# Optimization experiments

Hardware: AMD Instinct MI355X
Metric: run time of the kernel (lower is better)

## Reference

```python
import jax, jax.numpy as jnp
import numpy as np

EPS = 1e-9


def setup_inputs() -> dict:
    key = jax.random.key(0)
    k1, k2, k3 = jax.random.split(key, 3)
    B, N, E, F_IN, F_OUT = 8, 2048, 1024, 256, 256
    x = jax.random.normal(k1, (B, N, F_IN), dtype=jnp.float32)
    H = jax.random.uniform(k2, (B, N, E), dtype=jnp.float32)  # soft incidence matrix
    weight = jax.random.normal(k3, (F_IN, F_OUT), dtype=jnp.float32) * (1.0 / np.sqrt(F_OUT))
    return {"x": x, "H": H, "weight": weight}


def reference(x, H, weight):
    # x: [B, N, Fin], H: [B, N, E], weight: [Fin, Fout]
    # Torch builds diag_embed(Dv_inv)/diag_embed(De_inv) and uses dense bmm;
    # mathematically identical to elementwise row-scaling, done here directly.
    Dv = jnp.sum(H, axis=2)                       # [B, N]  (= bmm(H, ones))
    De = jnp.sum(H, axis=1)                       # [B, E]
    Dv_inv = 1.0 / (Dv + EPS)
    De_inv = 1.0 / (De + EPS)
    xw = jnp.matmul(x, weight)                    # [B, N, Fout]
    HTX = jnp.einsum('bne,bnf->bef', H, xw)       # H^T @ X
    HDeHTX = jnp.einsum('bne,bef->bnf', H, De_inv[:, :, None] * HTX)
    out = Dv_inv[:, :, None] * HDeHTX             # [B, N, Fout]
    # dropout in eval mode (identity); relu kept
    return jax.nn.relu(out)
```

## Files before the change

### kernel.cpp

```cpp
#include <hip/hip_runtime.h>
#include <stdint.h>


typedef __bf16 bf16x8 __attribute__((ext_vector_type(8)));
typedef float f32x4 __attribute__((ext_vector_type(4)));

#define PADK 72

__device__ __forceinline__ uint16_t f2b(float f) {
  __bf16 h = (__bf16)f;
  return __builtin_bit_cast(uint16_t, h);
}

__device__ __forceinline__ f32x4 mfma16(bf16x8 a, bf16x8 b, f32x4 c) {
  return __builtin_amdgcn_mfma_f32_16x16x32_bf16(a, b, c, 0, 0, 0);
}

__device__ __forceinline__ void gload16(const void* src, void* dst) {
  __builtin_amdgcn_global_load_lds(
      (const __attribute__((address_space(1))) void*)src,
      (__attribute__((address_space(3))) void*)dst, 16, 0, 0);
}

#define PIPE_WAIT4() do { \
    asm volatile("s_waitcnt vmcnt(4)" ::: "memory"); \
    __builtin_amdgcn_s_barrier(); \
    __builtin_amdgcn_sched_barrier(0); \
  } while (0)
#define PIPE_WAIT0() do { \
    asm volatile("s_waitcnt vmcnt(0)" ::: "memory"); \
    __builtin_amdgcn_s_barrier(); \
    __builtin_amdgcn_sched_barrier(0); \
  } while (0)

__global__ __launch_bounds__(256) void k_prep_w(const float* __restrict__ W,
    uint16_t* __restrict__ Wt) {
  __shared__ __align__(16) uint16_t T[64 * 68];
  const int k0 = blockIdx.x * 64, f0 = blockIdx.y * 64;
  const int t = threadIdx.x;
  const int r0 = (t >> 4) * 4, cc = (t & 15) * 4;
  float vv[4][4];
  #pragma unroll
  for (int i = 0; i < 4; ++i) {
    float4 q = *(const float4*)(W + (size_t)(k0 + r0 + i) * 256 + f0 + cc);
    vv[i][0] = q.x; vv[i][1] = q.y; vv[i][2] = q.z; vv[i][3] = q.w;
  }
  #pragma unroll
  for (int j = 0; j < 4; ++j) {
    union { uint16_t s[4]; uint2 u; } p;
    #pragma unroll
    for (int i = 0; i < 4; ++i) p.s[i] = f2b(vv[i][j]);
    *(uint2*)&T[(cc + j) * 68 + r0] = p.u;
  }
  __syncthreads();
  const int er = t >> 2, c2 = (t & 3) * 16;
  union { uint16_t s[16]; uint4 q[2]; } o;
  #pragma unroll
  for (int m = 0; m < 4; ++m)
    *(uint2*)&o.s[m * 4] = *(const uint2*)&T[er * 68 + c2 + m * 4];
  uint16_t* dst = Wt + (size_t)(f0 + er) * 256 + k0 + c2;
  *(uint4*)dst = o.q[0];
  *(uint4*)(dst + 8) = o.q[1];
}

__global__ __launch_bounds__(256) void k_prep_h(const float* __restrict__ H,
    uint16_t* __restrict__ Hbt, uint16_t* __restrict__ Hb,
    float* __restrict__ DvPart, float* __restrict__ DePart) {
  __shared__ __align__(16) uint16_t T[64 * 68];
  __shared__ float cs[4][64];
  const int n0 = blockIdx.x * 64, e0 = blockIdx.y * 64, b = blockIdx.z;
  const int t = threadIdx.x, lane = t & 63, wave = t >> 6;
  const int r0 = (t >> 4) * 4;
  const int cc = (t & 15) * 4;
  float vv[4][4];
  float dv[4];
  float de0 = 0.f, de1 = 0.f, de2 = 0.f, de3 = 0.f;
  #pragma unroll
  for (int i = 0; i < 4; ++i) {
    float4 q = *(const float4*)(H + ((size_t)b * 2048 + n0 + r0 + i) * 1024 + e0 + cc);
    vv[i][0] = q.x; vv[i][1] = q.y; vv[i][2] = q.z; vv[i][3] = q.w;
    float rs = (q.x + q.y) + (q.z + q.w);
    rs += __shfl_xor(rs, 1); rs += __shfl_xor(rs, 2);
    rs += __shfl_xor(rs, 4); rs += __shfl_xor(rs, 8);
    dv[i] = rs;
    de0 += q.x; de1 += q.y; de2 += q.z; de3 += q.w;
  }
  #pragma unroll
  for (int i = 0; i < 4; ++i) {
    union { uint16_t s[4]; uint2 u; } p;
    #pragma unroll
    for (int j = 0; j < 4; ++j) p.s[j] = f2b(vv[i][j]);
    *(uint2*)(Hb + ((size_t)b * 2048 + n0 + r0 + i) * 1024 + e0 + cc) = p.u;
  }
  #pragma unroll
  for (int j = 0; j < 4; ++j) {
    union { uint16_t s[4]; uint2 u; } p;
    #pragma unroll
    for (int i = 0; i < 4; ++i) p.s[i] = f2b(vv[i][j]);
    *(uint2*)&T[(cc + j) * 68 + r0] = p.u;
  }
  de0 += __shfl_xor(de0, 16); de0 += __shfl_xor(de0, 32);
  de1 += __shfl_xor(de1, 16); de1 += __shfl_xor(de1, 32);
  de2 += __shfl_xor(de2, 16); de2 += __shfl_xor(de2, 32);
  de3 += __shfl_xor(de3, 16); de3 += __shfl_xor(de3, 32);
  if (lane < 16) *(float4*)&cs[wave][cc] = make_float4(de0, de1, de2, de3);
  if ((lane & 15) == 0) {
    #pragma unroll
    for (int i = 0; i < 4; ++i)
      DvPart[((size_t)b * 2048 + n0 + r0 + i) * 16 + blockIdx.y] = dv[i];
  }
  __syncthreads();
  const int er = t >> 2, c2 = (t & 3) * 16;
  union { uint16_t s[16]; uint4 q[2]; } o;
  #pragma unroll
  for (int m = 0; m < 4; ++m)
    *(uint2*)&o.s[m * 4] = *(const uint2*)&T[er * 68 + c2 + m * 4];
  uint16_t* dst = Hbt + ((size_t)b * 1024 + e0 + er) * 2048 + n0 + c2;
  *(uint4*)dst = o.q[0];
  *(uint4*)(dst + 8) = o.q[1];
  if (t < 64) {
    float s = (cs[0][t] + cs[1][t]) + (cs[2][t] + cs[3][t]);
    DePart[((size_t)b * 1024 + e0 + t) * 32 + blockIdx.x] = s;
  }
}

__global__ __launch_bounds__(256) void k_gemm1(const float* __restrict__ X,
    const uint16_t* __restrict__ Wt, uint16_t* __restrict__ XWt) {
  __shared__ __align__(16) uint16_t As[2][128 * 64];
  __shared__ __align__(16) uint16_t Bs[2][64 * PADK];
  const int n0 = blockIdx.x * 64, f0 = blockIdx.y * 128, b = blockIdx.z;
  const int t = threadIdx.x, lane = t & 63, wave = t >> 6;
  const int l15 = lane & 15, lq = lane >> 4;
  const int rlane = lane >> 3;
  const int srcswz = ((lane & 7) ^ rlane) << 3;
  const uint16_t* Ag = Wt + (size_t)f0 * 256;
  const int br = t >> 2, kc = (t & 3) * 16;
  const float* Xg = X + ((size_t)b * 2048 + n0 + br) * 256 + kc;
  float4 RX[4];
  auto stageA = [&](uint16_t* Ad, int kt) {
    const int k0 = kt * 64;
    #pragma unroll
    for (int i = 0; i < 4; ++i) {
      const int r = wave * 32 + i * 8;
      gload16(Ag + (size_t)(r + rlane) * 256 + k0 + srcswz, Ad + r * 64);
    }
  };
  auto gloadB = [&](int kt) {
    const float* s = Xg + kt * 64;
    #pragma unroll
    for (int q = 0; q < 4; ++q) RX[q] = *(const float4*)(s + q * 4);
  };
  auto writeB = [&](uint16_t* Bd) {
    uint16_t* d = Bd + br * PADK + kc;
    const float* f = (const float*)RX;
    #pragma unroll
    for (int q = 0; q < 2; ++q) {
      union { uint16_t s[8]; uint4 u; } p;
      #pragma unroll
      for (int j = 0; j < 8; ++j) p.s[j] = f2b(f[q * 8 + j]);
      *(uint4*)(d + q * 8) = p.u;
    }
  };
  f32x4 acc[4][2] = {};
  auto compute = [&](const uint16_t* Ad, const uint16_t* Bd) {
    #pragma unroll
    for (int h = 0; h < 2; ++h) {
      bf16x8 af[4], bf[2];
      #pragma unroll
      for (int i = 0; i < 4; ++i) {
        const int r = (wave >> 1) * 64 + i * 16 + l15;
        af[i] = *(const bf16x8*)(Ad + r * 64 + ((((h << 2) | lq) ^ (r & 7)) << 3));
      }
      #pragma unroll
      for (int j = 0; j < 2; ++j) {
        const int r = (wave & 1) * 32 + j * 16 + l15;
        bf[j] = *(const bf16x8*)(Bd + r * PADK + h * 32 + lq * 8);
      }
      #pragma unroll
      for (int i = 0; i < 4; ++i)
        #pragma unroll
        for (int j = 0; j < 2; ++j)
          acc[i][j] = mfma16(af[i], bf[j], acc[i][j]);
    }
  };
  stageA(As[0], 0); gloadB(0); writeB(Bs[0]);
  __syncthreads();
  for (int kt = 0; kt < 4; kt += 2) {
    stageA(As[1], kt + 1); gloadB(kt + 1);
    compute(As[0], Bs[0]);
    writeB(Bs[1]);
    __syncthreads();
    if (kt + 2 < 4) { stageA(As[0], kt + 2); gloadB(kt + 2); }
    compute(As[1], Bs[1]);
    if (kt + 2 < 4) writeB(Bs[0]);
    __syncthreads();
  }
  #pragma unroll
  for (int i = 0; i < 4; ++i) {
    const int fr = f0 + (wave >> 1) * 64 + i * 16 + lq * 4;
    #pragma unroll
    for (int j = 0; j < 2; ++j) {
      const int col = n0 + (wave & 1) * 32 + j * 16 + l15;
      #pragma unroll
      for (int reg = 0; reg < 4; ++reg)
        XWt[((size_t)b * 256 + fr + reg) * 2048 + col] = f2b(acc[i][j][reg]);
    }
  }
}

__global__ __launch_bounds__(256) void k_gemm2(const uint16_t* __restrict__ Hbt,
    const uint16_t* __restrict__ XWt, const float* __restrict__ DePart,
    uint16_t* __restrict__ Yt) {
  __shared__ __align__(16) uint16_t As[3][64 * 64];
  __shared__ __align__(16) uint16_t Bs[3][64 * 64];
  __shared__ float sde[64];
  const int e0 = blockIdx.x * 64, f0 = blockIdx.y * 64, b = blockIdx.z;
  const int t = threadIdx.x, lane = t & 63, wave = t >> 6;
  const int l15 = lane & 15, lq = lane >> 4;
  const int rlane = lane >> 3;
  const int srcswz = ((lane & 7) ^ rlane) << 3;
  const uint16_t* Ag = XWt + ((size_t)b * 256 + f0) * 2048;
  const uint16_t* Bg = Hbt + ((size_t)b * 1024 + e0) * 2048;
  auto stage = [&](uint16_t* Ad, uint16_t* Bd, int kt) {
    const int k0 = kt * 64;
    #pragma unroll
    for (int i = 0; i < 2; ++i) {
      const int r = wave * 16 + i * 8;
      gload16(Ag + (size_t)(r + rlane) * 2048 + k0 + srcswz, Ad + r * 64);
      gload16(Bg + (size_t)(r + rlane) * 2048 + k0 + srcswz, Bd + r * 64);
    }
  };
  f32x4 acc[2][2] = {};
  auto compute = [&](const uint16_t* Ad, const uint16_t* Bd) {
    #pragma unroll
    for (int h = 0; h < 2; ++h) {
      bf16x8 af[2], bf[2];
      #pragma unroll
      for (int i = 0; i < 2; ++i) {
        const int r = (wave >> 1) * 32 + i * 16 + l15;
        af[i] = *(const bf16x8*)(Ad + r * 64 + ((((h << 2) | lq) ^ (r & 7)) << 3));
      }
      #pragma unroll
      for (int j = 0; j < 2; ++j) {
        const int r = (wave & 1) * 32 + j * 16 + l15;
        bf[j] = *(const bf16x8*)(Bd + r * 64 + ((((h << 2) | lq) ^ (r & 7)) << 3));
      }
      #pragma unroll
      for (int i = 0; i < 2; ++i)
        #pragma unroll
        for (int j = 0; j < 2; ++j)
          acc[i][j] = mfma16(af[i], bf[j], acc[i][j]);
    }
  };
  if (t < 64) {
    const float* p = DePart + ((size_t)b * 1024 + e0 + t) * 32;
    float4 a0 = *(const float4*)(p + 0),  a1 = *(const float4*)(p + 4);
    float4 a2 = *(const float4*)(p + 8),  a3 = *(const float4*)(p + 12);
    float4 a4 = *(const float4*)(p + 16), a5 = *(const float4*)(p + 20);
    float4 a6 = *(const float4*)(p + 24), a7 = *(const float4*)(p + 28);
    float s = (((a0.x + a0.y) + (a0.z + a0.w)) + ((a1.x + a1.y) + (a1.z + a1.w)))
            + (((a2.x + a2.y) + (a2.z + a2.w)) + ((a3.x + a3.y) + (a3.z + a3.w)))
            + ((((a4.x + a4.y) + (a4.z + a4.w)) + ((a5.x + a5.y) + (a5.z + a5.w)))
            + (((a6.x + a6.y) + (a6.z + a6.w)) + ((a7.x + a7.y) + (a7.z + a7.w))));
    sde[t] = 1.f / (s + 1e-9f);
  }
  stage(As[0], Bs[0], 0);
  stage(As[1], Bs[1], 1);
  __syncthreads();
  const int NT = 32;
  uint16_t *cA = As[0], *nA = As[1], *fA = As[2];
  uint16_t *cB = Bs[0], *nB = Bs[1], *fB = Bs[2];
  for (int kt = 0; kt < NT - 2; ++kt) {
    stage(fA, fB, kt + 2);
    compute(cA, cB);
    PIPE_WAIT4();
    uint16_t* t1 = cA; cA = nA; nA = fA; fA = t1;
    uint16_t* t2 = cB; cB = nB; nB = fB; fB = t2;
  }
  compute(cA, cB);
  PIPE_WAIT0();
  compute(nA, nB);
  #pragma unroll
  for (int i = 0; i < 2; ++i) {
    const int fr = f0 + (wave >> 1) * 32 + i * 16 + lq * 4;
    #pragma unroll
    for (int j = 0; j < 2; ++j) {
      const int el = (wave & 1) * 32 + j * 16 + l15;
      const float sc = sde[el];
      uint16_t* dst = Yt + ((size_t)b * 256 + fr) * 1024 + e0 + el;
      #pragma unroll
      for (int reg = 0; reg < 4; ++reg)
        dst[(size_t)reg * 1024] = f2b(acc[i][j][reg] * sc);
    }
  }
}

__global__ __launch_bounds__(256) void k_gemm3(const uint16_t* __restrict__ Hb,
    const uint16_t* __restrict__ Yt, const float* __restrict__ DvPart,
    float* __restrict__ out) {
  __shared__ __align__(16) uint16_t As[3][64 * 64];
  __shared__ __align__(16) uint16_t Bs[3][64 * 64];
  __shared__ float sdv[64];
  const int n0 = blockIdx.x * 64, f0 = blockIdx.y * 64, b = blockIdx.z;
  const int t = threadIdx.x, lane = t & 63, wave = t >> 6;
  const int l15 = lane & 15, lq = lane >> 4;
  const int rlane = lane >> 3;
  const int srcswz = ((lane & 7) ^ rlane) << 3;
  const uint16_t* Ag = Hb + ((size_t)b * 2048 + n0) * 1024;
  const uint16_t* Bg = Yt + ((size_t)b * 256 + f0) * 1024;
  auto stage = [&](uint16_t* Ad, uint16_t* Bd, int kt) {
    const int k0 = kt * 64;
    #pragma unroll
    for (int i = 0; i < 2; ++i) {
      const int r = wave * 16 + i * 8;
      gload16(Ag + (size_t)(r + rlane) * 1024 + k0 + srcswz, Ad + r * 64);
      gload16(Bg + (size_t)(r + rlane) * 1024 + k0 + srcswz, Bd + r * 64);
    }
  };
  f32x4 acc[2][2] = {};
  auto compute = [&](const uint16_t* Ad, const uint16_t* Bd) {
    #pragma unroll
    for (int h = 0; h < 2; ++h) {
      bf16x8 af[2], bf[2];
      #pragma unroll
      for (int i = 0; i < 2; ++i) {
        const int r = (wave >> 1) * 32 + i * 16 + l15;
        af[i] = *(const bf16x8*)(Ad + r * 64 + ((((h << 2) | lq) ^ (r & 7)) << 3));
      }
      #pragma unroll
      for (int j = 0; j < 2; ++j) {
        const int r = (wave & 1) * 32 + j * 16 + l15;
        bf[j] = *(const bf16x8*)(Bd + r * 64 + ((((h << 2) | lq) ^ (r & 7)) << 3));
      }
      #pragma unroll
      for (int i = 0; i < 2; ++i)
        #pragma unroll
        for (int j = 0; j < 2; ++j)
          acc[i][j] = mfma16(af[i], bf[j], acc[i][j]);
    }
  };
  if (t < 64) {
    const float* p = DvPart + ((size_t)b * 2048 + n0 + t) * 16;
    float4 a0 = *(const float4*)(p + 0),  a1 = *(const float4*)(p + 4);
    float4 a2 = *(const float4*)(p + 8),  a3 = *(const float4*)(p + 12);
    float s = (((a0.x + a0.y) + (a0.z + a0.w)) + ((a1.x + a1.y) + (a1.z + a1.w)))
            + (((a2.x + a2.y) + (a2.z + a2.w)) + ((a3.x + a3.y) + (a3.z + a3.w)));
    sdv[t] = 1.f / (s + 1e-9f);
  }
  stage(As[0], Bs[0], 0);
  stage(As[1], Bs[1], 1);
  __syncthreads();
  const int NT = 16;
  uint16_t *cA = As[0], *nA = As[1], *fA = As[2];
  uint16_t *cB = Bs[0], *nB = Bs[1], *fB = Bs[2];
  for (int kt = 0; kt < NT - 2; ++kt) {
    stage(fA, fB, kt + 2);
    compute(cA, cB);
    PIPE_WAIT4();
    uint16_t* t1 = cA; cA = nA; nA = fA; fA = t1;
    uint16_t* t2 = cB; cB = nB; nB = fB; fB = t2;
  }
  compute(cA, cB);
  PIPE_WAIT0();
  compute(nA, nB);
  #pragma unroll
  for (int i = 0; i < 2; ++i) {
    const int nl = (wave >> 1) * 32 + i * 16 + lq * 4;
    #pragma unroll
    for (int reg = 0; reg < 4; ++reg) {
      const int row = n0 + nl + reg;
      const float sc = sdv[nl + reg];
      #pragma unroll
      for (int j = 0; j < 2; ++j) {
        const int col = f0 + (wave & 1) * 32 + j * 16 + l15;
        const float v = acc[i][j][reg] * sc;
        out[((size_t)b * 2048 + row) * 256 + col] = v > 0.f ? v : 0.f;
      }
    }
  }
}

extern "C" void kernel_launch(void* const* d_in, const int* in_sizes, int n_in,
                              void* d_out, int out_size, void* d_ws, size_t ws_size,
                              hipStream_t stream) {
  (void)in_sizes; (void)n_in; (void)out_size;
  const float* x = (const float*)d_in[0];
  const float* H = (const float*)d_in[1];
  const float* W = (const float*)d_in[2];
  float* out = (float*)d_out;

  if (ws_size < 81920000) return;
  char* ws = (char*)d_ws;
  uint16_t* Hbt    = (uint16_t*)(ws);
  uint16_t* Hb     = (uint16_t*)(ws + 33554432);
  uint16_t* XWt    = (uint16_t*)(ws + 67108864);
  uint16_t* Yt     = (uint16_t*)(ws + 75497472);
  float*    DvPart = (float*)(ws + 79691776);
  float*    DePart = (float*)(ws + 80740352);
  uint16_t* Wt     = (uint16_t*)(ws + 81788928);

  k_prep_w<<<dim3(4, 4),      256, 0, stream>>>(W, Wt);
  k_prep_h<<<dim3(32, 16, 8), 256, 0, stream>>>(H, Hbt, Hb, DvPart, DePart);
  k_gemm1 <<<dim3(32, 2, 8),  256, 0, stream>>>(x, Wt, XWt);
  k_gemm2 <<<dim3(16, 4, 8),  256, 0, stream>>>(Hbt, XWt, DePart, Yt);
  k_gemm3 <<<dim3(32, 4, 8),  256, 0, stream>>>(Hb, Yt, DvPart, out);
}
```

Measured before the change: 79.37 us.

## Enlarge GEMM2 and GEMM3 tiles with K=32 stages and new swizzle

GEMM2 now has each 512-thread block cover the full 256-wide feature dimension for a 64-edge tile, so the H tile is loaded once rather than four times. GEMM3 moves to 128x128 output tiles with 4x4 MFMA accumulators per wave. Both kernels drop the K step to 32 with a matching LDS swizzle and adjust the pipeline wait counts to fit. Operand reuse per global load goes up, but grids shrink a lot: GEMM2 drops to 128 blocks and GEMM3 to 256. That may underfill the GPU's CUs and add latency exposure per block.

```diff
diff --git a/kernel.cpp b/kernel.cpp
--- a/kernel.cpp
+++ b/kernel.cpp
@@ -22,13 +22,8 @@
       (__attribute__((address_space(3))) void*)dst, 16, 0, 0);
 }
 
-#define PIPE_WAIT4() do { \
-    asm volatile("s_waitcnt vmcnt(4)" ::: "memory"); \
-    __builtin_amdgcn_s_barrier(); \
-    __builtin_amdgcn_sched_barrier(0); \
-  } while (0)
-#define PIPE_WAIT0() do { \
-    asm volatile("s_waitcnt vmcnt(0)" ::: "memory"); \
+#define PIPE_WAITN(N) do { \
+    asm volatile("s_waitcnt vmcnt(" #N ")" ::: "memory"); \
     __builtin_amdgcn_s_barrier(); \
     __builtin_amdgcn_sched_barrier(0); \
   } while (0)
@@ -208,49 +203,46 @@
   }
 }
 
-__global__ __launch_bounds__(256) void k_gemm2(const uint16_t* __restrict__ Hbt,
+__global__ __launch_bounds__(512) void k_gemm2(const uint16_t* __restrict__ Hbt,
     const uint16_t* __restrict__ XWt, const float* __restrict__ DePart,
     uint16_t* __restrict__ Yt) {
-  __shared__ __align__(16) uint16_t As[3][64 * 64];
-  __shared__ __align__(16) uint16_t Bs[3][64 * 64];
+  __shared__ __align__(16) uint16_t As[3][256 * 32];
+  __shared__ __align__(16) uint16_t Bs[3][64 * 32];
   __shared__ float sde[64];
-  const int e0 = blockIdx.x * 64, f0 = blockIdx.y * 64, b = blockIdx.z;
+  const int e0 = blockIdx.x * 64, b = blockIdx.z;
   const int t = threadIdx.x, lane = t & 63, wave = t >> 6;
   const int l15 = lane & 15, lq = lane >> 4;
-  const int rlane = lane >> 3;
-  const int srcswz = ((lane & 7) ^ rlane) << 3;
-  const uint16_t* Ag = XWt + ((size_t)b * 256 + f0) * 2048;
+  const int wf = wave >> 1, we = wave & 1;
+  const int ri = lane >> 2, slot = lane & 3;
+  const int ksw = (slot ^ ((ri >> 1) & 3)) * 8;
+  const uint16_t* Ag = XWt + (size_t)b * 256 * 2048;
   const uint16_t* Bg = Hbt + ((size_t)b * 1024 + e0) * 2048;
   auto stage = [&](uint16_t* Ad, uint16_t* Bd, int kt) {
-    const int k0 = kt * 64;
-    #pragma unroll
-    for (int i = 0; i < 2; ++i) {
-      const int r = wave * 16 + i * 8;
-      gload16(Ag + (size_t)(r + rlane) * 2048 + k0 + srcswz, Ad + r * 64);
-      gload16(Bg + (size_t)(r + rlane) * 2048 + k0 + srcswz, Bd + r * 64);
-    }
-  };
-  f32x4 acc[2][2] = {};
+    const int k0 = kt * 32;
+    const int a0 = wave * 2;
+    gload16(Ag + (size_t)(a0 * 16 + ri) * 2048 + k0 + ksw, Ad + a0 * 512);
+    gload16(Ag + (size_t)(a0 * 16 + 16 + ri) * 2048 + k0 + ksw, Ad + (a0 + 1) * 512);
+    const int bb = wave >> 1;
+    gload16(Bg + (size_t)(bb * 16 + ri) * 2048 + k0 + ksw, Bd + bb * 512);
+  };
+  f32x4 acc[4][2] = {};
   auto compute = [&](const uint16_t* Ad, const uint16_t* Bd) {
-    #pragma unroll
-    for (int h = 0; h < 2; ++h) {
-      bf16x8 af[2], bf[2];
-      #pragma unroll
-      for (int i = 0; i < 2; ++i) {
-        const int r = (wave >> 1) * 32 + i * 16 + l15;
-        af[i] = *(const bf16x8*)(Ad + r * 64 + ((((h << 2) | lq) ^ (r & 7)) << 3));
-      }
-      #pragma unroll
-      for (int j = 0; j < 2; ++j) {
-        const int r = (wave & 1) * 32 + j * 16 + l15;
-        bf[j] = *(const bf16x8*)(Bd + r * 64 + ((((h << 2) | lq) ^ (r & 7)) << 3));
-      }
-      #pragma unroll
-      for (int i = 0; i < 2; ++i)
-        #pragma unroll
-        for (int j = 0; j < 2; ++j)
-          acc[i][j] = mfma16(af[i], bf[j], acc[i][j]);
-    }
+    bf16x8 af[4], bf[2];
+    #pragma unroll
+    for (int i = 0; i < 4; ++i) {
+      const int r = wf * 64 + i * 16 + l15;
+      af[i] = *(const bf16x8*)(Ad + r * 32 + ((lq ^ ((r >> 1) & 3)) * 8));
+    }
+    #pragma unroll
+    for (int j = 0; j < 2; ++j) {
+      const int r = we * 32 + j * 16 + l15;
+      bf[j] = *(const bf16x8*)(Bd + r * 32 + ((lq ^ ((r >> 1) & 3)) * 8));
+    }
+    #pragma unroll
+    for (int i = 0; i < 4; ++i)
+      #pragma unroll
+      for (int j = 0; j < 2; ++j)
+        acc[i][j] = mfma16(af[i], bf[j], acc[i][j]);
   };
   if (t < 64) {
     const float* p = DePart + ((size_t)b * 1024 + e0 + t) * 32;
@@ -267,112 +259,110 @@
   stage(As[0], Bs[0], 0);
   stage(As[1], Bs[1], 1);
   __syncthreads();
+  const int NT = 64;
+  uint16_t *cA = As[0], *nA = As[1], *fA = As[2];
+  uint16_t *cB = Bs[0], *nB = Bs[1], *fB = Bs[2];
+  for (int kt = 0; kt < NT - 2; ++kt) {
+    stage(fA, fB, kt + 2);
+    compute(cA, cB);
+    PIPE_WAITN(3);
+    uint16_t* t1 = cA; cA = nA; nA = fA; fA = t1;
+    uint16_t* t2 = cB; cB = nB; nB = fB; fB = t2;
+  }
+  compute(cA, cB);
+  PIPE_WAITN(0);
+  compute(nA, nB);
+  #pragma unroll
+  for (int i = 0; i < 4; ++i) {
+    const int fr = wf * 64 + i * 16 + lq * 4;
+    #pragma unroll
+    for (int j = 0; j < 2; ++j) {
+      const int el = we * 32 + j * 16 + l15;
+      const float sc = sde[el];
+      uint16_t* dst = Yt + ((size_t)b * 256 + fr) * 1024 + e0 + el;
+      #pragma unroll
+      for (int reg = 0; reg < 4; ++reg)
+        dst[(size_t)reg * 1024] = f2b(acc[i][j][reg] * sc);
+    }
+  }
+}
+
+__global__ __launch_bounds__(256) void k_gemm3(const uint16_t* __restrict__ Hb,
+    const uint16_t* __restrict__ Yt, const float* __restrict__ DvPart,
+    float* __restrict__ out) {
+  __shared__ __align__(16) uint16_t As[3][128 * 32];
+  __shared__ __align__(16) uint16_t Bs[3][128 * 32];
+  __shared__ float sdv[128];
+  const int n0 = blockIdx.x * 128, f0 = blockIdx.y * 128, b = blockIdx.z;
+  const int t = threadIdx.x, lane = t & 63, wave = t >> 6;
+  const int l15 = lane & 15, lq = lane >> 4;
+  const int wn = wave >> 1, wf = wave & 1;
+  const int ri = lane >> 2, slot = lane & 3;
+  const int ksw = (slot ^ ((ri >> 1) & 3)) * 8;
+  const uint16_t* Ag = Hb + ((size_t)b * 2048 + n0) * 1024;
+  const uint16_t* Bg = Yt + ((size_t)b * 256 + f0) * 1024;
+  auto stage = [&](uint16_t* Ad, uint16_t* Bd, int kt) {
+    const int k0 = kt * 32;
+    const int c0 = wave * 2;
+    #pragma unroll
+    for (int i = 0; i < 2; ++i) {
+      gload16(Ag + (size_t)((c0 + i) * 16 + ri) * 1024 + k0 + ksw, Ad + (c0 + i) * 512);
+      gload16(Bg + (size_t)((c0 + i) * 16 + ri) * 1024 + k0 + ksw, Bd + (c0 + i) * 512);
+    }
+  };
+  f32x4 acc[4][4] = {};
+  auto compute = [&](const uint16_t* Ad, const uint16_t* Bd) {
+    bf16x8 af[4], bf[4];
+    #pragma unroll
+    for (int i = 0; i < 4; ++i) {
+      const int r = wn * 64 + i * 16 + l15;
+      af[i] = *(const bf16x8*)(Ad + r * 32 + ((lq ^ ((r >> 1) & 3)) * 8));
+    }
+    #pragma unroll
+    for (int j = 0; j < 4; ++j) {
+      const int r = wf * 64 + j * 16 + l15;
+      bf[j] = *(const bf16x8*)(Bd + r * 32 + ((lq ^ ((r >> 1) & 3)) * 8));
+    }
+    #pragma unroll
+    for (int i = 0; i < 4; ++i)
+      #pragma unroll
+      for (int j = 0; j < 4; ++j)
+        acc[i][j] = mfma16(af[i], bf[j], acc[i][j]);
+  };
+  if (t < 128) {
+    const float* p = DvPart + ((size_t)b * 2048 + n0 + t) * 16;
+    float4 a0 = *(const float4*)(p + 0),  a1 = *(const float4*)(p + 4);
+    float4 a2 = *(const float4*)(p + 8),  a3 = *(const float4*)(p + 12);
+    float s = (((a0.x + a0.y) + (a0.z + a0.w)) + ((a1.x + a1.y) + (a1.z + a1.w)))
+            + (((a2.x + a2.y) + (a2.z + a2.w)) + ((a3.x + a3.y) + (a3.z + a3.w)));
+    sdv[t] = 1.f / (s + 1e-9f);
+  }
+  stage(As[0], Bs[0], 0);
+  stage(As[1], Bs[1], 1);
+  __syncthreads();
   const int NT = 32;
   uint16_t *cA = As[0], *nA = As[1], *fA = As[2];
   uint16_t *cB = Bs[0], *nB = Bs[1], *fB = Bs[2];
   for (int kt = 0; kt < NT - 2; ++kt) {
     stage(fA, fB, kt + 2);
     compute(cA, cB);
-    PIPE_WAIT4();
+    PIPE_WAITN(4);
     uint16_t* t1 = cA; cA = nA; nA = fA; fA = t1;
     uint16_t* t2 = cB; cB = nB; nB = fB; fB = t2;
   }
   compute(cA, cB);
-  PIPE_WAIT0();
+  PIPE_WAITN(0);
   compute(nA, nB);
   #pragma unroll
-  for (int i = 0; i < 2; ++i) {
-    const int fr = f0 + (wave >> 1) * 32 + i * 16 + lq * 4;
-    #pragma unroll
-    for (int j = 0; j < 2; ++j) {
-      const int el = (wave & 1) * 32 + j * 16 + l15;
-      const float sc = sde[el];
-      uint16_t* dst = Yt + ((size_t)b * 256 + fr) * 1024 + e0 + el;
-      #pragma unroll
-      for (int reg = 0; reg < 4; ++reg)
-        dst[(size_t)reg * 1024] = f2b(acc[i][j][reg] * sc);
-    }
-  }
-}
-
-__global__ __launch_bounds__(256) void k_gemm3(const uint16_t* __restrict__ Hb,
-    const uint16_t* __restrict__ Yt, const float* __restrict__ DvPart,
-    float* __restrict__ out) {
-  __shared__ __align__(16) uint16_t As[3][64 * 64];
-  __shared__ __align__(16) uint16_t Bs[3][64 * 64];
-  __shared__ float sdv[64];
-  const int n0 = blockIdx.x * 64, f0 = blockIdx.y * 64, b = blockIdx.z;
-  const int t = threadIdx.x, lane = t & 63, wave = t >> 6;
-  const int l15 = lane & 15, lq = lane >> 4;
-  const int rlane = lane >> 3;
-  const int srcswz = ((lane & 7) ^ rlane) << 3;
-  const uint16_t* Ag = Hb + ((size_t)b * 2048 + n0) * 1024;
-  const uint16_t* Bg = Yt + ((size_t)b * 256 + f0) * 1024;
-  auto stage = [&](uint16_t* Ad, uint16_t* Bd, int kt) {
-    const int k0 = kt * 64;
-    #pragma unroll
-    for (int i = 0; i < 2; ++i) {
-      const int r = wave * 16 + i * 8;
-      gload16(Ag + (size_t)(r + rlane) * 1024 + k0 + srcswz, Ad + r * 64);
-      gload16(Bg + (size_t)(r + rlane) * 1024 + k0 + srcswz, Bd + r * 64);
-    }
-  };
-  f32x4 acc[2][2] = {};
-  auto compute = [&](const uint16_t* Ad, const uint16_t* Bd) {
-    #pragma unroll
-    for (int h = 0; h < 2; ++h) {
-      bf16x8 af[2], bf[2];
-      #pragma unroll
-      for (int i = 0; i < 2; ++i) {
-        const int r = (wave >> 1) * 32 + i * 16 + l15;
-        af[i] = *(const bf16x8*)(Ad + r * 64 + ((((h << 2) | lq) ^ (r & 7)) << 3));
-      }
-      #pragma unroll
-      for (int j = 0; j < 2; ++j) {
-        const int r = (wave & 1) * 32 + j * 16 + l15;
-        bf[j] = *(const bf16x8*)(Bd + r * 64 + ((((h << 2) | lq) ^ (r & 7)) << 3));
-      }
-      #pragma unroll
-      for (int i = 0; i < 2; ++i)
-        #pragma unroll
-        for (int j = 0; j < 2; ++j)
-          acc[i][j] = mfma16(af[i], bf[j], acc[i][j]);
-    }
-  };
-  if (t < 64) {
-    const float* p = DvPart + ((size_t)b * 2048 + n0 + t) * 16;
-    float4 a0 = *(const float4*)(p + 0),  a1 = *(const float4*)(p + 4);
-    float4 a2 = *(const float4*)(p + 8),  a3 = *(const float4*)(p + 12);
-    float s = (((a0.x + a0.y) + (a0.z + a0.w)) + ((a1.x + a1.y) + (a1.z + a1.w)))
-            + (((a2.x + a2.y) + (a2.z + a2.w)) + ((a3.x + a3.y) + (a3.z + a3.w)));
-    sdv[t] = 1.f / (s + 1e-9f);
-  }
-  stage(As[0], Bs[0], 0);
-  stage(As[1], Bs[1], 1);
-  __syncthreads();
-  const int NT = 16;
-  uint16_t *cA = As[0], *nA = As[1], *fA = As[2];
-  uint16_t *cB = Bs[0], *nB = Bs[1], *fB = Bs[2];
-  for (int kt = 0; kt < NT - 2; ++kt) {
-    stage(fA, fB, kt + 2);
-    compute(cA, cB);
-    PIPE_WAIT4();
-    uint16_t* t1 = cA; cA = nA; nA = fA; fA = t1;
-    uint16_t* t2 = cB; cB = nB; nB = fB; fB = t2;
-  }
-  compute(cA, cB);
-  PIPE_WAIT0();
-  compute(nA, nB);
-  #pragma unroll
-  for (int i = 0; i < 2; ++i) {
-    const int nl = (wave >> 1) * 32 + i * 16 + lq * 4;
+  for (int i = 0; i < 4; ++i) {
+    const int nl = wn * 64 + i * 16 + lq * 4;
     #pragma unroll
     for (int reg = 0; reg < 4; ++reg) {
       const int row = n0 + nl + reg;
       const float sc = sdv[nl + reg];
       #pragma unroll
-      for (int j = 0; j < 2; ++j) {
-        const int col = f0 + (wave & 1) * 32 + j * 16 + l15;
+      for (int j = 0; j < 4; ++j) {
+        const int col = f0 + wf * 64 + j * 16 + l15;
         const float v = acc[i][j][reg] * sc;
         out[((size_t)b * 2048 + row) * 256 + col] = v > 0.f ? v : 0.f;
       }
@@ -402,6 +392,6 @@
   k_prep_w<<<dim3(4, 4),      256, 0, stream>>>(W, Wt);
   k_prep_h<<<dim3(32, 16, 8), 256, 0, stream>>>(H, Hbt, Hb, DvPart, DePart);
   k_gemm1 <<<dim3(32, 2, 8),  256, 0, stream>>>(x, Wt, XWt);
-  k_gemm2 <<<dim3(16, 4, 8),  256, 0, stream>>>(Hbt, XWt, DePart, Yt);
-  k_gemm3 <<<dim3(32, 4, 8),  256, 0, stream>>>(Hb, Yt, DvPart, out);
-}
+  k_gemm2 <<<dim3(16, 1, 8),  512, 0, stream>>>(Hbt, XWt, DePart, Yt);
+  k_gemm3 <<<dim3(16, 2, 8),  256, 0, stream>>>(Hb, Yt, DvPart, out);
+}
```

Result: slower. 92.38 us (+16.4%).

## Merge H preprocessing and X·W GEMM into one heterogeneous launch

Applied to the files above, without the earlier changes.

Folds the H conversion/degree kernel and the X·W GEMM into one kernel whose first 512 blocks do the GEMM and whose remaining 4096 blocks do the H work. This removes a launch boundary and lets the compute-heavy GEMM blocks run alongside the memory-bound H blocks. In exchange, the GEMM loses its double-buffered LDS pipeline and now syncs twice per k-step. Both block types share one 25.6KB shared buffer, which may affect occupancy for the H blocks.

```diff
diff --git a/kernel.cpp b/kernel.cpp
--- a/kernel.cpp
+++ b/kernel.cpp
@@ -63,147 +63,137 @@
   *(uint4*)(dst + 8) = o.q[1];
 }
 
-__global__ __launch_bounds__(256) void k_prep_h(const float* __restrict__ H,
+__global__ __launch_bounds__(256) void k_phase1(const float* __restrict__ H,
+    const float* __restrict__ X, const uint16_t* __restrict__ Wt,
     uint16_t* __restrict__ Hbt, uint16_t* __restrict__ Hb,
-    float* __restrict__ DvPart, float* __restrict__ DePart) {
-  __shared__ __align__(16) uint16_t T[64 * 68];
-  __shared__ float cs[4][64];
-  const int n0 = blockIdx.x * 64, e0 = blockIdx.y * 64, b = blockIdx.z;
+    float* __restrict__ DvPart, float* __restrict__ DePart,
+    uint16_t* __restrict__ XWt) {
+  __shared__ __align__(16) unsigned char smem[25600];
+  const int lin = blockIdx.x;
   const int t = threadIdx.x, lane = t & 63, wave = t >> 6;
-  const int r0 = (t >> 4) * 4;
-  const int cc = (t & 15) * 4;
-  float vv[4][4];
-  float dv[4];
-  float de0 = 0.f, de1 = 0.f, de2 = 0.f, de3 = 0.f;
-  #pragma unroll
-  for (int i = 0; i < 4; ++i) {
-    float4 q = *(const float4*)(H + ((size_t)b * 2048 + n0 + r0 + i) * 1024 + e0 + cc);
-    vv[i][0] = q.x; vv[i][1] = q.y; vv[i][2] = q.z; vv[i][3] = q.w;
-    float rs = (q.x + q.y) + (q.z + q.w);
-    rs += __shfl_xor(rs, 1); rs += __shfl_xor(rs, 2);
-    rs += __shfl_xor(rs, 4); rs += __shfl_xor(rs, 8);
-    dv[i] = rs;
-    de0 += q.x; de1 += q.y; de2 += q.z; de3 += q.w;
-  }
-  #pragma unroll
-  for (int i = 0; i < 4; ++i) {
-    union { uint16_t s[4]; uint2 u; } p;
-    #pragma unroll
-    for (int j = 0; j < 4; ++j) p.s[j] = f2b(vv[i][j]);
-    *(uint2*)(Hb + ((size_t)b * 2048 + n0 + r0 + i) * 1024 + e0 + cc) = p.u;
-  }
-  #pragma unroll
-  for (int j = 0; j < 4; ++j) {
-    union { uint16_t s[4]; uint2 u; } p;
-    #pragma unroll
-    for (int i = 0; i < 4; ++i) p.s[i] = f2b(vv[i][j]);
-    *(uint2*)&T[(cc + j) * 68 + r0] = p.u;
-  }
-  de0 += __shfl_xor(de0, 16); de0 += __shfl_xor(de0, 32);
-  de1 += __shfl_xor(de1, 16); de1 += __shfl_xor(de1, 32);
-  de2 += __shfl_xor(de2, 16); de2 += __shfl_xor(de2, 32);
-  de3 += __shfl_xor(de3, 16); de3 += __shfl_xor(de3, 32);
-  if (lane < 16) *(float4*)&cs[wave][cc] = make_float4(de0, de1, de2, de3);
-  if ((lane & 15) == 0) {
-    #pragma unroll
-    for (int i = 0; i < 4; ++i)
-      DvPart[((size_t)b * 2048 + n0 + r0 + i) * 16 + blockIdx.y] = dv[i];
-  }
-  __syncthreads();
-  const int er = t >> 2, c2 = (t & 3) * 16;
-  union { uint16_t s[16]; uint4 q[2]; } o;
-  #pragma unroll
-  for (int m = 0; m < 4; ++m)
-    *(uint2*)&o.s[m * 4] = *(const uint2*)&T[er * 68 + c2 + m * 4];
-  uint16_t* dst = Hbt + ((size_t)b * 1024 + e0 + er) * 2048 + n0 + c2;
-  *(uint4*)dst = o.q[0];
-  *(uint4*)(dst + 8) = o.q[1];
-  if (t < 64) {
-    float s = (cs[0][t] + cs[1][t]) + (cs[2][t] + cs[3][t]);
-    DePart[((size_t)b * 1024 + e0 + t) * 32 + blockIdx.x] = s;
-  }
-}
-
-__global__ __launch_bounds__(256) void k_gemm1(const float* __restrict__ X,
-    const uint16_t* __restrict__ Wt, uint16_t* __restrict__ XWt) {
-  __shared__ __align__(16) uint16_t As[2][128 * 64];
-  __shared__ __align__(16) uint16_t Bs[2][64 * PADK];
-  const int n0 = blockIdx.x * 64, f0 = blockIdx.y * 128, b = blockIdx.z;
-  const int t = threadIdx.x, lane = t & 63, wave = t >> 6;
-  const int l15 = lane & 15, lq = lane >> 4;
-  const int rlane = lane >> 3;
-  const int srcswz = ((lane & 7) ^ rlane) << 3;
-  const uint16_t* Ag = Wt + (size_t)f0 * 256;
-  const int br = t >> 2, kc = (t & 3) * 16;
-  const float* Xg = X + ((size_t)b * 2048 + n0 + br) * 256 + kc;
-  float4 RX[4];
-  auto stageA = [&](uint16_t* Ad, int kt) {
-    const int k0 = kt * 64;
+
+  if (lin < 512) {
+    uint16_t* As = (uint16_t*)smem;
+    uint16_t* Bs = (uint16_t*)(smem + 16384);
+    const int n0 = (lin & 31) * 64, f0 = ((lin >> 5) & 1) * 128, b = lin >> 6;
+    const int l15 = lane & 15, lq = lane >> 4;
+    const int rlane = lane >> 3;
+    const int srcswz = ((lane & 7) ^ rlane) << 3;
+    const uint16_t* Ag = Wt + (size_t)f0 * 256;
+    const int br = t >> 2, kc = (t & 3) * 16;
+    const float* Xg = X + ((size_t)b * 2048 + n0 + br) * 256 + kc;
+    f32x4 acc[4][2] = {};
+    for (int kt = 0; kt < 4; ++kt) {
+      if (kt) __syncthreads();
+      const int k0 = kt * 64;
+      #pragma unroll
+      for (int i = 0; i < 4; ++i) {
+        const int r = wave * 32 + i * 8;
+        gload16(Ag + (size_t)(r + rlane) * 256 + k0 + srcswz, As + r * 64);
+      }
+      {
+        float4 RX[4];
+        const float* s = Xg + k0;
+        #pragma unroll
+        for (int q = 0; q < 4; ++q) RX[q] = *(const float4*)(s + q * 4);
+        uint16_t* d = Bs + br * PADK + kc;
+        const float* f = (const float*)RX;
+        #pragma unroll
+        for (int q = 0; q < 2; ++q) {
+          union { uint16_t s[8]; uint4 u; } p;
+          #pragma unroll
+          for (int j = 0; j < 8; ++j) p.s[j] = f2b(f[q * 8 + j]);
+          *(uint4*)(d + q * 8) = p.u;
+        }
+      }
+      __syncthreads();
+      #pragma unroll
+      for (int h = 0; h < 2; ++h) {
+        bf16x8 af[4], bf[2];
+        #pragma unroll
+        for (int i = 0; i < 4; ++i) {
+          const int r = (wave >> 1) * 64 + i * 16 + l15;
+          af[i] = *(const bf16x8*)(As + r * 64 + ((((h << 2) | lq) ^ (r & 7)) << 3));
+        }
+        #pragma unroll
+        for (int j = 0; j < 2; ++j) {
+          const int r = (wave & 1) * 32 + j * 16 + l15;
+          bf[j] = *(const bf16x8*)(Bs + r * PADK + h * 32 + lq * 8);
+        }
+        #pragma unroll
+        for (int i = 0; i < 4; ++i)
+          #pragma unroll
+          for (int j = 0; j < 2; ++j)
+            acc[i][j] = mfma16(af[i], bf[j], acc[i][j]);
+      }
+    }
     #pragma unroll
     for (int i = 0; i < 4; ++i) {
-      const int r = wave * 32 + i * 8;
-      gload16(Ag + (size_t)(r + rlane) * 256 + k0 + srcswz, Ad + r * 64);
-    }
-  };
-  auto gloadB = [&](int kt) {
-    const float* s = Xg + kt * 64;
-    #pragma unroll
-    for (int q = 0; q < 4; ++q) RX[q] = *(const float4*)(s + q * 4);
-  };
-  auto writeB = [&](uint16_t* Bd) {
-    uint16_t* d = Bd + br * PADK + kc;
-    const float* f = (const float*)RX;
-    #pragma unroll
-    for (int q = 0; q < 2; ++q) {
-      union { uint16_t s[8]; uint4 u; } p;
-      #pragma unroll
-      for (int j = 0; j < 8; ++j) p.s[j] = f2b(f[q * 8 + j]);
-      *(uint4*)(d + q * 8) = p.u;
-    }
-  };
-  f32x4 acc[4][2] = {};
-  auto compute = [&](const uint16_t* Ad, const uint16_t* Bd) {
-    #pragma unroll
-    for (int h = 0; h < 2; ++h) {
-      bf16x8 af[4], bf[2];
-      #pragma unroll
-      for (int i = 0; i < 4; ++i) {
-        const int r = (wave >> 1) * 64 + i * 16 + l15;
-        af[i] = *(const bf16x8*)(Ad + r * 64 + ((((h << 2) | lq) ^ (r & 7)) << 3));
-      }
+      const int fr = f0 + (wave >> 1) * 64 + i * 16 + lq * 4;
       #pragma unroll
       for (int j = 0; j < 2; ++j) {
-        const int r = (wave & 1) * 32 + j * 16 + l15;
-        bf[j] = *(const bf16x8*)(Bd + r * PADK + h * 32 + lq * 8);
-      }
+        const int col = n0 + (wave & 1) * 32 + j * 16 + l15;
+        #pragma unroll
+        for (int reg = 0; reg < 4; ++reg)
+          XWt[((size_t)b * 256 + fr + reg) * 2048 + col] = f2b(acc[i][j][reg]);
+      }
+    }
+  } else {
+    uint16_t* T = (uint16_t*)smem;
+    float* cs = (float*)(smem + 8704);
+    const int l2 = lin - 512;
+    const int n0 = (l2 & 31) * 64, e0 = ((l2 >> 5) & 15) * 64, b = l2 >> 9;
+    const int r0 = (t >> 4) * 4;
+    const int cc = (t & 15) * 4;
+    float vv[4][4];
+    float dv[4];
+    float de0 = 0.f, de1 = 0.f, de2 = 0.f, de3 = 0.f;
+    #pragma unroll
+    for (int i = 0; i < 4; ++i) {
+      float4 q = *(const float4*)(H + ((size_t)b * 2048 + n0 + r0 + i) * 1024 + e0 + cc);
+      vv[i][0] = q.x; vv[i][1] = q.y; vv[i][2] = q.z; vv[i][3] = q.w;
+      float rs = (q.x + q.y) + (q.z + q.w);
+      rs += __shfl_xor(rs, 1); rs += __shfl_xor(rs, 2);
+      rs += __shfl_xor(rs, 4); rs += __shfl_xor(rs, 8);
+      dv[i] = rs;
+      de0 += q.x; de1 += q.y; de2 += q.z; de3 += q.w;
+    }
+    #pragma unroll
+    for (int i = 0; i < 4; ++i) {
+      union { uint16_t s[4]; uint2 u; } p;
+      #pragma unroll
+      for (int j = 0; j < 4; ++j) p.s[j] = f2b(vv[i][j]);
+      *(uint2*)(Hb + ((size_t)b * 2048 + n0 + r0 + i) * 1024 + e0 + cc) = p.u;
+    }
+    #pragma unroll
+    for (int j = 0; j < 4; ++j) {
+      union { uint16_t s[4]; uint2 u; } p;
+      #pragma unroll
+      for (int i = 0; i < 4; ++i) p.s[i] = f2b(vv[i][j]);
+      *(uint2*)&T[(cc + j) * 68 + r0] = p.u;
+    }
+    de0 += __shfl_xor(de0, 16); de0 += __shfl_xor(de0, 32);
+    de1 += __shfl_xor(de1, 16); de1 += __shfl_xor(de1, 32);
+    de2 += __shfl_xor(de2, 16); de2 += __shfl_xor(de2, 32);
+    de3 += __shfl_xor(de3, 16); de3 += __shfl_xor(de3, 32);
+    if (lane < 16) *(float4*)&cs[wave * 64 + cc] = make_float4(de0, de1, de2, de3);
+    if ((lane & 15) == 0) {
       #pragma unroll
       for (int i = 0; i < 4; ++i)
-        #pragma unroll
-        for (int j = 0; j < 2; ++j)
-          acc[i][j] = mfma16(af[i], bf[j], acc[i][j]);
-    }
-  };
-  stageA(As[0], 0); gloadB(0); writeB(Bs[0]);
-  __syncthreads();
-  for (int kt = 0; kt < 4; kt += 2) {
-    stageA(As[1], kt + 1); gloadB(kt + 1);
-    compute(As[0], Bs[0]);
-    writeB(Bs[1]);
+        DvPart[((size_t)b * 2048 + n0 + r0 + i) * 16 + ((l2 >> 5) & 15)] = dv[i];
+    }
     __syncthreads();
-    if (kt + 2 < 4) { stageA(As[0], kt + 2); gloadB(kt + 2); }
-    compute(As[1], Bs[1]);
-    if (kt + 2 < 4) writeB(Bs[0]);
-    __syncthreads();
-  }
-  #pragma unroll
-  for (int i = 0; i < 4; ++i) {
-    const int fr = f0 + (wave >> 1) * 64 + i * 16 + lq * 4;
-    #pragma unroll
-    for (int j = 0; j < 2; ++j) {
-      const int col = n0 + (wave & 1) * 32 + j * 16 + l15;
-      #pragma unroll
-      for (int reg = 0; reg < 4; ++reg)
-        XWt[((size_t)b * 256 + fr + reg) * 2048 + col] = f2b(acc[i][j][reg]);
+    const int er = t >> 2, c2 = (t & 3) * 16;
+    union { uint16_t s[16]; uint4 q[2]; } o;
+    #pragma unroll
+    for (int m = 0; m < 4; ++m)
+      *(uint2*)&o.s[m * 4] = *(const uint2*)&T[er * 68 + c2 + m * 4];
+    uint16_t* dst = Hbt + ((size_t)b * 1024 + e0 + er) * 2048 + n0 + c2;
+    *(uint4*)dst = o.q[0];
+    *(uint4*)(dst + 8) = o.q[1];
+    if (t < 64) {
+      float s = (cs[0 * 64 + t] + cs[1 * 64 + t]) + (cs[2 * 64 + t] + cs[3 * 64 + t]);
+      DePart[((size_t)b * 1024 + e0 + t) * 32 + (l2 & 31)] = s;
     }
   }
 }
@@ -399,9 +389,8 @@
   float*    DePart = (float*)(ws + 80740352);
   uint16_t* Wt     = (uint16_t*)(ws + 81788928);
 
-  k_prep_w<<<dim3(4, 4),      256, 0, stream>>>(W, Wt);
-  k_prep_h<<<dim3(32, 16, 8), 256, 0, stream>>>(H, Hbt, Hb, DvPart, DePart);
-  k_gemm1 <<<dim3(32, 2, 8),  256, 0, stream>>>(x, Wt, XWt);
-  k_gemm2 <<<dim3(16, 4, 8),  256, 0, stream>>>(Hbt, XWt, DePart, Yt);
-  k_gemm3 <<<dim3(32, 4, 8),  256, 0, stream>>>(Hb, Yt, DvPart, out);
-}
+  k_prep_w<<<dim3(4, 4),     256, 0, stream>>>(W, Wt);
+  k_phase1<<<dim3(4608),     256, 0, stream>>>(H, x, Wt, Hbt, Hb, DvPart, DePart, XWt);
+  k_gemm2 <<<dim3(16, 4, 8), 256, 0, stream>>>(Hbt, XWt, DePart, Yt);
+  k_gemm3 <<<dim3(32, 4, 8), 256, 0, stream>>>(Hb, Yt, DvPart, out);
+}
```

Result: faster. 76.46 us, median of 2 (-3.7%).
